# Kernel tuning notes

Measured on AMD Instinct MI355X. Metric: run time of the kernel, lower is better.

Reference implementation:

```python
import jax, jax.numpy as jnp
import numpy as np

EPS = 1e-5

def layer_norm(x, w, b):
    mu = jnp.mean(x, axis=-1, keepdims=True)
    var = jnp.mean(jnp.square(x - mu), axis=-1, keepdims=True)
    return (x - mu) * jax.lax.rsqrt(var + EPS) * w + b

def setup_inputs() -> dict:
    key = jax.random.key(0)
    ks = jax.random.split(key, 16)
    B, N, c_z, c_h = 1, 512, 128, 128
    s_z = 1.0 / np.sqrt(c_z)
    s_h = 1.0 / np.sqrt(c_h)
    return {
        "z": jax.random.normal(ks[0], (B, N, N, c_z), jnp.float32),
        "mask": jnp.ones((B, N, N), jnp.float32),
        "norm_in_w": jnp.ones((c_z,), jnp.float32),
        "norm_in_b": jnp.zeros((c_z,), jnp.float32),
        "a_p_w": jax.random.normal(ks[1], (c_h, c_z), jnp.float32) * s_z,
        "a_p_b": jnp.zeros((c_h,), jnp.float32),
        "a_g_w": jax.random.normal(ks[2], (c_h, c_z), jnp.float32) * s_z,
        "a_g_b": jnp.ones((c_h,), jnp.float32),
        "b_p_w": jax.random.normal(ks[3], (c_h, c_z), jnp.float32) * s_z,
        "b_p_b": jnp.zeros((c_h,), jnp.float32),
        "b_g_w": jax.random.normal(ks[4], (c_h, c_z), jnp.float32) * s_z,
        "b_g_b": jnp.ones((c_h,), jnp.float32),
        "g_w": jax.random.normal(ks[5], (c_z, c_z), jnp.float32) * s_z,
        "g_b": jnp.ones((c_z,), jnp.float32),
        "z_w": jax.random.normal(ks[6], (c_z, c_h), jnp.float32) * s_h,
        "z_b": jnp.zeros((c_z,), jnp.float32),
        "norm_out_w": jnp.ones((c_h,), jnp.float32),
        "norm_out_b": jnp.zeros((c_h,), jnp.float32),
    }

OUTGOING = True

def reference(z, mask, norm_in_w, norm_in_b, a_p_w, a_p_b, a_g_w, a_g_b,
              b_p_w, b_p_b, b_g_w, b_g_b, g_w, g_b, z_w, z_b,
              norm_out_w, norm_out_b):
    # z: [B, N, N, c_z]; mask: [B, N, N]
    m = mask[..., None]  # [B, N, N, 1]
    zn = layer_norm(z, norm_in_w, norm_in_b)
    # gated projections (nn.Linear layout: W is [out, in])
    a = m * jax.nn.sigmoid(zn @ a_g_w.T + a_g_b) * (zn @ a_p_w.T + a_p_b)
    b = m * jax.nn.sigmoid(zn @ b_g_w.T + b_g_b) * (zn @ b_p_w.T + b_p_b)
    if OUTGOING:
        # x[i,j,c] = sum_k a[i,k,c] * b[j,k,c]
        x = jnp.einsum('bikc,bjkc->bijc', a, b)
    else:
        x = jnp.einsum('bkic,bkjc->bijc', a, b)
    x = layer_norm(x, norm_out_w, norm_out_b)
    x = x @ z_w.T + z_b
    g = jax.nn.sigmoid(zn @ g_w.T + g_b)
    return x * g
```

## Files before the change

kernel.cpp:

```cpp
#include <hip/hip_runtime.h>
#include <stddef.h>

#define NN 512
#define CC 128
#define NPOS (NN*NN)
#define CPITCH (NPOS + 512)

typedef unsigned short u16;
typedef unsigned int   u32;
typedef u16  u16x4  __attribute__((ext_vector_type(4)));
typedef u16  u16x8  __attribute__((ext_vector_type(8)));
typedef __bf16 bf16x8 __attribute__((ext_vector_type(8)));
typedef float f32x4  __attribute__((ext_vector_type(4)));

__device__ __forceinline__ float b2f(u16 u) {
    union { u32 i; float f; } w; w.i = ((u32)u) << 16; return w.f;
}
__device__ __forceinline__ u16 f2b(float f) {
    return __builtin_bit_cast(u16, (__bf16)f);
}
__device__ __forceinline__ float sigm(float x) { return 1.0f / (1.0f + __expf(-x)); }

__device__ __forceinline__ void gld16(const u16* g, u16* l) {
    __builtin_amdgcn_global_load_lds(
        (const __attribute__((address_space(1))) u32*)g,
        (__attribute__((address_space(3))) u32*)l, 16, 0, 0);
}

struct W6 { const float* p[6]; };

__global__ __launch_bounds__(256) void k0_pack(W6 w, u16* __restrict__ dst)
{
    const int i = blockIdx.x * 256 + threadIdx.x;
    const int mt = i >> 14, r = i & 16383;
    const int cb = r >> 11, ks = (r >> 9) & 3, lane = (r >> 3) & 63, j = r & 7;
    const int row = cb * 16 + (lane & 15);
    const int col = ks * 32 + (lane >> 4) * 8 + j;
    dst[i] = f2b(w.p[mt][row * 128 + col]);
}

__global__ __launch_bounds__(128) void k1_ln_proj(
    const float* __restrict__ z,  const float* __restrict__ mask,
    const float* __restrict__ wi, const float* __restrict__ bi,
    const u16* __restrict__ wpk,
    const float* __restrict__ agb, const float* __restrict__ apb,
    const float* __restrict__ bgb, const float* __restrict__ bpb,
    u16* __restrict__ a_cm, u16* __restrict__ b_cm)
{
    __shared__ u16 zn[64][136];
    const int tid = threadIdx.x;
    const size_t p0 = (size_t)blockIdx.x * 64;

    {
        const float* zt = z + p0 * CC;
        const int g  = tid >> 5;
        const int c4 = (tid & 31) * 4;
        const f32x4 wi4 = *(const f32x4*)(wi + c4);
        const f32x4 bi4 = *(const f32x4*)(bi + c4);
        f32x4 v[16];
        #pragma unroll
        for (int h = 0; h < 16; ++h)
            v[h] = *(const f32x4*)(zt + h * 512 + tid * 4);
        #pragma unroll
        for (int h = 0; h < 16; ++h) {
            float s  = (v[h][0] + v[h][1]) + (v[h][2] + v[h][3]);
            float s2 = (v[h][0]*v[h][0] + v[h][1]*v[h][1])
                     + (v[h][2]*v[h][2] + v[h][3]*v[h][3]);
            #pragma unroll
            for (int ms = 1; ms <= 16; ms <<= 1) {
                s  += __shfl_xor(s,  ms);
                s2 += __shfl_xor(s2, ms);
            }
            const float mu   = s * (1.0f / CC);
            const float rstd = rsqrtf(s2 * (1.0f / CC) - mu * mu + 1e-5f);
            u16x4 o4;
            #pragma unroll
            for (int e = 0; e < 4; ++e) {
                const float nw = rstd * wi4[e];
                o4[e] = f2b(v[h][e] * nw + __builtin_fmaf(-mu, nw, bi4[e]));
            }
            *(u16x4*)&zn[h * 4 + g][c4] = o4;
        }
    }
    __syncthreads();

    const int wave = tid >> 6, lane = tid & 63;
    const int m = lane & 15, q = lane >> 4;

    bf16x8 af[2][4];
    #pragma unroll
    for (int t = 0; t < 2; ++t)
        #pragma unroll
        for (int ks = 0; ks < 4; ++ks)
            af[t][ks] = *(const bf16x8*)&zn[wave * 32 + t * 16 + m][ks * 32 + q * 8];

    f32x4 mkv[2];
    #pragma unroll
    for (int t = 0; t < 2; ++t)
        mkv[t] = *(const f32x4*)(mask + p0 + wave * 32 + t * 16 + q * 4);

    const float* Bv[4] = { agb, apb, bgb, bpb };

    for (int cb = 0; cb < 8; ++cb) {
        const int o = cb * 16 + m;
        f32x4 res[4][2];
        #pragma unroll
        for (int mt = 0; mt < 4; ++mt) {
            const float bvv = Bv[mt][o];
            #pragma unroll
            for (int t = 0; t < 2; ++t) res[mt][t] = f32x4{ bvv, bvv, bvv, bvv };
            const u16* wp = wpk + ((size_t)((mt * 8 + cb) * 4)) * 512 + (size_t)lane * 8;
            bf16x8 wf[4];
            #pragma unroll
            for (int ks = 0; ks < 4; ++ks) wf[ks] = *(const bf16x8*)(wp + ks * 512);
            #pragma unroll
            for (int ks = 0; ks < 4; ++ks)
                #pragma unroll
                for (int t = 0; t < 2; ++t)
                    res[mt][t] = __builtin_amdgcn_mfma_f32_16x16x32_bf16(
                                   af[t][ks], wf[ks], res[mt][t], 0, 0, 0);
        }
        #pragma unroll
        for (int t = 0; t < 2; ++t) {
            u16x4 av, bv;
            #pragma unroll
            for (int r = 0; r < 4; ++r) {
                const float mk = mkv[t][r];
                av[r] = f2b(mk * sigm(res[0][t][r]) * res[1][t][r]);
                bv[r] = f2b(mk * sigm(res[2][t][r]) * res[3][t][r]);
            }
            const size_t off = (size_t)o * CPITCH + p0 + wave * 32 + t * 16 + q * 4;
            *(u16x4*)(a_cm + off) = av;
            *(u16x4*)(b_cm + off) = bv;
        }
    }
}

__global__ __launch_bounds__(256) void k2_gemm(
    const u16* __restrict__ A, const u16* __restrict__ B, u16* __restrict__ X)
{
    __shared__ u16 As[2][128][32];
    __shared__ u16 Bs[2][128][32];
    const int tid = threadIdx.x;
    const int bx  = blockIdx.x;
    const int c   = bx >> 4;
    const int i0  = ((bx >> 2) & 3) * 128;
    const int j0  = (bx & 3) * 128;
    const size_t cbase = (size_t)c * CPITCH;
    const u16* Ac = A + cbase;
    const u16* Bc = B + cbase;

    const int wave = tid >> 6, lane = tid & 63;
    const int wm = wave >> 1, wn = wave & 1;
    const int m = lane & 15, q = lane >> 4;

    f32x4 acc[4][4];
    const f32x4 zero = { 0.f, 0.f, 0.f, 0.f };
    #pragma unroll
    for (int mt = 0; mt < 4; ++mt)
        #pragma unroll
        for (int nt = 0; nt < 4; ++nt) acc[mt][nt] = zero;

    for (int kt = 0; kt < 8; ++kt) {
        __syncthreads();
        #pragma unroll
        for (int ps = 0; ps < 4; ++ps) {
            const int id   = ps * 256 + tid;
            const int half = id >> 9;
            const int rw   = (id >> 2) & 127;
            const int g    = (id & 3) ^ ((rw >> 1) & 3);
            const size_t goff = (size_t)(kt * 64 + half * 32 + g * 8);
            gld16(Ac + (size_t)(i0 + rw) * NN + goff, &As[0][0][0] + id * 8);
            gld16(Bc + (size_t)(j0 + rw) * NN + goff, &Bs[0][0][0] + id * 8);
        }
        __syncthreads();
        #pragma unroll
        for (int ks = 0; ks < 2; ++ks) {
            bf16x8 af[4], bf[4];
            #pragma unroll
            for (int mt = 0; mt < 4; ++mt) {
                const int row = wm * 64 + mt * 16 + m;
                const int slot = q ^ ((row >> 1) & 3);
                af[mt] = *(const bf16x8*)&As[ks][row][slot * 8];
            }
            #pragma unroll
            for (int nt = 0; nt < 4; ++nt) {
                const int row = wn * 64 + nt * 16 + m;
                const int slot = q ^ ((row >> 1) & 3);
                bf[nt] = *(const bf16x8*)&Bs[ks][row][slot * 8];
            }
            #pragma unroll
            for (int mt = 0; mt < 4; ++mt)
                #pragma unroll
                for (int nt = 0; nt < 4; ++nt)
                    acc[mt][nt] = __builtin_amdgcn_mfma_f32_16x16x32_bf16(
                                    af[mt], bf[nt], acc[mt][nt], 0, 0, 0);
        }
    }

    #pragma unroll
    for (int mt = 0; mt < 4; ++mt) {
        #pragma unroll
        for (int r = 0; r < 4; ++r) {
            const int i = i0 + wm * 64 + mt * 16 + q * 4 + r;
            #pragma unroll
            for (int nt = 0; nt < 4; ++nt) {
                const int j = j0 + wn * 64 + nt * 16 + m;
                X[cbase + (size_t)i * NN + j] = f2b(acc[mt][nt][r]);
            }
        }
    }
}

__global__ __launch_bounds__(256) void k3_out(
    float* __restrict__ out, const u16* __restrict__ x_cm,
    const float* __restrict__ z,
    const float* __restrict__ wi, const float* __restrict__ bi,
    const float* __restrict__ wo, const float* __restrict__ bo,
    const u16* __restrict__ wpk,
    const float* __restrict__ gbv, const float* __restrict__ zbv)
{
    __shared__ u16 A[128][136];
    __shared__ u16 Bt[128][136];
    const int tid = threadIdx.x;
    const size_t p0 = (size_t)blockIdx.x * 128;
    const int wave = tid >> 6, lane = tid & 63;
    const int m = lane & 15, q = lane >> 4;
    const int pl = tid >> 1, ht = tid & 1;

    {
        const float* zr = z + (p0 + pl) * CC + ht * 64;
        float v[64];
        #pragma unroll
        for (int h = 0; h < 16; ++h) {
            f32x4 t = *(const f32x4*)(zr + h * 4);
            #pragma unroll
            for (int e = 0; e < 4; ++e) v[h * 4 + e] = t[e];
        }
        float s = 0.f, s2 = 0.f;
        #pragma unroll
        for (int e = 0; e < 64; ++e) { s += v[e]; s2 += v[e] * v[e]; }
        s  += __shfl_xor(s, 1);
        s2 += __shfl_xor(s2, 1);
        const float mu   = s * (1.0f / CC);
        const float rstd = rsqrtf(s2 * (1.0f / CC) - mu * mu + 1e-5f);
        #pragma unroll
        for (int h = 0; h < 8; ++h) {
            u16x8 o8;
            #pragma unroll
            for (int e = 0; e < 8; ++e) {
                const int c = ht * 64 + h * 8 + e;
                o8[e] = f2b((v[h * 8 + e] - mu) * rstd * wi[c] + bi[c]);
            }
            *(u16x8*)&A[pl][ht * 64 + h * 8] = o8;
        }
    }
    {
        const int c = tid >> 1, seg = tid & 1;
        #pragma unroll
        for (int e = 0; e < 8; ++e) {
            u16x8 vv = *(const u16x8*)(x_cm + (size_t)c * CPITCH + p0 + seg * 64 + e * 8);
            *(u16x8*)&Bt[c][seg * 64 + e * 8] = vv;
        }
    }
    __syncthreads();

    bf16x8 afz[2][4];
    #pragma unroll
    for (int t = 0; t < 2; ++t)
        #pragma unroll
        for (int ks = 0; ks < 4; ++ks)
            afz[t][ks] = *(const bf16x8*)&A[wave * 32 + t * 16 + m][ks * 32 + q * 8];
    __syncthreads();

    {
        float v[64];
        #pragma unroll
        for (int e = 0; e < 64; ++e) v[e] = b2f(Bt[ht * 64 + e][pl]);
        float s = 0.f, s2 = 0.f;
        #pragma unroll
        for (int e = 0; e < 64; ++e) { s += v[e]; s2 += v[e] * v[e]; }
        s  += __shfl_xor(s, 1);
        s2 += __shfl_xor(s2, 1);
        const float mu   = s * (1.0f / CC);
        const float rstd = rsqrtf(s2 * (1.0f / CC) - mu * mu + 1e-5f);
        #pragma unroll
        for (int h = 0; h < 8; ++h) {
            u16x8 o8;
            #pragma unroll
            for (int e = 0; e < 8; ++e) {
                const int c = ht * 64 + h * 8 + e;
                o8[e] = f2b((v[h * 8 + e] - mu) * rstd * wo[c] + bo[c]);
            }
            *(u16x8*)&A[pl][ht * 64 + h * 8] = o8;
        }
    }
    __syncthreads();

    bf16x8 afx[2][4];
    #pragma unroll
    for (int t = 0; t < 2; ++t)
        #pragma unroll
        for (int ks = 0; ks < 4; ++ks)
            afx[t][ks] = *(const bf16x8*)&A[wave * 32 + t * 16 + m][ks * 32 + q * 8];

    for (int cb = 0; cb < 8; ++cb) {
        const int o = cb * 16 + m;
        const float gb0 = gbv[o], zb0 = zbv[o];
        f32x4 accg[2], accx[2];
        #pragma unroll
        for (int t = 0; t < 2; ++t) {
            accg[t] = f32x4{ gb0, gb0, gb0, gb0 };
            accx[t] = f32x4{ zb0, zb0, zb0, zb0 };
        }
        const u16* wpg = wpk + ((size_t)((4 * 8 + cb) * 4)) * 512 + (size_t)lane * 8;
        const u16* wpz = wpk + ((size_t)((5 * 8 + cb) * 4)) * 512 + (size_t)lane * 8;
        bf16x8 wg[4], wz[4];
        #pragma unroll
        for (int ks = 0; ks < 4; ++ks) {
            wg[ks] = *(const bf16x8*)(wpg + ks * 512);
            wz[ks] = *(const bf16x8*)(wpz + ks * 512);
        }
        #pragma unroll
        for (int ks = 0; ks < 4; ++ks)
            #pragma unroll
            for (int t = 0; t < 2; ++t) {
                accg[t] = __builtin_amdgcn_mfma_f32_16x16x32_bf16(
                            afz[t][ks], wg[ks], accg[t], 0, 0, 0);
                accx[t] = __builtin_amdgcn_mfma_f32_16x16x32_bf16(
                            afx[t][ks], wz[ks], accx[t], 0, 0, 0);
            }
        #pragma unroll
        for (int t = 0; t < 2; ++t)
            #pragma unroll
            for (int r = 0; r < 4; ++r) {
                const size_t p = p0 + wave * 32 + t * 16 + q * 4 + r;
                out[p * CC + o] = accx[t][r] * sigm(accg[t][r]);
            }
    }
}

extern "C" void kernel_launch(void* const* d_in, const int* in_sizes, int n_in,
                              void* d_out, int out_size, void* d_ws, size_t ws_size,
                              hipStream_t stream)
{
    const float* z    = (const float*)d_in[0];
    const float* mask = (const float*)d_in[1];
    const float* wi   = (const float*)d_in[2];
    const float* bi   = (const float*)d_in[3];
    const float* apw  = (const float*)d_in[4];
    const float* apb  = (const float*)d_in[5];
    const float* agw  = (const float*)d_in[6];
    const float* agb  = (const float*)d_in[7];
    const float* bpw  = (const float*)d_in[8];
    const float* bpb  = (const float*)d_in[9];
    const float* bgw  = (const float*)d_in[10];
    const float* bgb  = (const float*)d_in[11];
    const float* gw   = (const float*)d_in[12];
    const float* gb   = (const float*)d_in[13];
    const float* zw   = (const float*)d_in[14];
    const float* zb   = (const float*)d_in[15];
    const float* wo   = (const float*)d_in[16];
    const float* bo   = (const float*)d_in[17];

    u16* a_cm = (u16*)d_ws;
    u16* b_cm = a_cm + (size_t)CC * CPITCH;
    u16* x_cm = b_cm + (size_t)CC * CPITCH;
    u16* w_pk = x_cm + (size_t)CC * CPITCH;
    float* out = (float*)d_out;

    W6 w6; w6.p[0] = agw; w6.p[1] = apw; w6.p[2] = bgw; w6.p[3] = bpw;
    w6.p[4] = gw; w6.p[5] = zw;

    k0_pack<<<6 * 16384 / 256, 256, 0, stream>>>(w6, w_pk);
    k1_ln_proj<<<NPOS / 64, 128, 0, stream>>>(z, mask, wi, bi, w_pk,
                                              agb, apb, bgb, bpb, a_cm, b_cm);
    k2_gemm<<<128 * 16, 256, 0, stream>>>(a_cm, b_cm, x_cm);
    k3_out<<<NPOS / 128, 256, 0, stream>>>(out, x_cm, z, wi, bi, wo, bo,
                                           w_pk, gb, zb);
}
```

Measured before the change: 492.9 us.

## Cache bf16 normalized z for output stage and remap GEMM blocks across XCDs

The projection kernel now also writes the layer-normalized input as bf16 in position-major layout to workspace. A new output kernel reads it directly instead of re-reading fp32 z and recomputing the input layernorm, which halves that read traffic and drops redundant math at the cost of an extra 64 MB write. Separately, the channel GEMM's block-to-work mapping is changed so consecutive blocks on the same XCD share a channel, meant to improve L2 locality. The old path is kept as a fallback when the workspace is too small.

Measured after the change: 480.5 us. -2.5%, faster.

```diff
diff --git a/kernel.cpp b/kernel.cpp
--- a/kernel.cpp
+++ b/kernel.cpp
@@ -45,7 +45,8 @@
     const u16* __restrict__ wpk,
     const float* __restrict__ agb, const float* __restrict__ apb,
     const float* __restrict__ bgb, const float* __restrict__ bpb,
-    u16* __restrict__ a_cm, u16* __restrict__ b_cm)
+    u16* __restrict__ a_cm, u16* __restrict__ b_cm,
+    u16* __restrict__ zn_pm)
 {
     __shared__ u16 zn[64][136];
     const int tid = threadIdx.x;
@@ -80,6 +81,8 @@
                 o4[e] = f2b(v[h][e] * nw + __builtin_fmaf(-mu, nw, bi4[e]));
             }
             *(u16x4*)&zn[h * 4 + g][c4] = o4;
+            if (zn_pm)
+                *(u16x4*)(zn_pm + (p0 + h * 4 + g) * CC + c4) = o4;
         }
     }
     __syncthreads();
@@ -143,9 +146,12 @@
     __shared__ u16 Bs[2][128][32];
     const int tid = threadIdx.x;
     const int bx  = blockIdx.x;
-    const int c   = bx >> 4;
-    const int i0  = ((bx >> 2) & 3) * 128;
-    const int j0  = (bx & 3) * 128;
+    const int xcd  = bx & 7;
+    const int slot = bx >> 3;
+    const int c    = (slot >> 4) * 8 + xcd;
+    const int tile = slot & 15;
+    const int i0   = (tile >> 2) * 128;
+    const int j0   = (tile & 3) * 128;
     const size_t cbase = (size_t)c * CPITCH;
     const u16* Ac = A + cbase;
     const u16* Bc = B + cbase;
@@ -180,14 +186,14 @@
             #pragma unroll
             for (int mt = 0; mt < 4; ++mt) {
                 const int row = wm * 64 + mt * 16 + m;
-                const int slot = q ^ ((row >> 1) & 3);
-                af[mt] = *(const bf16x8*)&As[ks][row][slot * 8];
+                const int slt = q ^ ((row >> 1) & 3);
+                af[mt] = *(const bf16x8*)&As[ks][row][slt * 8];
             }
             #pragma unroll
             for (int nt = 0; nt < 4; ++nt) {
                 const int row = wn * 64 + nt * 16 + m;
-                const int slot = q ^ ((row >> 1) & 3);
-                bf[nt] = *(const bf16x8*)&Bs[ks][row][slot * 8];
+                const int slt = q ^ ((row >> 1) & 3);
+                bf[nt] = *(const bf16x8*)&Bs[ks][row][slt * 8];
             }
             #pragma unroll
             for (int mt = 0; mt < 4; ++mt)
@@ -209,6 +215,105 @@
                 X[cbase + (size_t)i * NN + j] = f2b(acc[mt][nt][r]);
             }
         }
+    }
+}
+
+__global__ __launch_bounds__(256) void k3_out_zn(
+    float* __restrict__ out, const u16* __restrict__ x_cm,
+    const u16* __restrict__ zn_pm,
+    const float* __restrict__ wo, const float* __restrict__ bo,
+    const u16* __restrict__ wpk,
+    const float* __restrict__ gbv, const float* __restrict__ zbv)
+{
+    __shared__ u16 A[128][136];
+    __shared__ u16 Bt[128][136];
+    const int tid = threadIdx.x;
+    const size_t p0 = (size_t)blockIdx.x * 128;
+    const int wave = tid >> 6, lane = tid & 63;
+    const int m = lane & 15, q = lane >> 4;
+    const int pl = tid >> 1, ht = tid & 1;
+
+    {
+        const int c = tid >> 1, seg = tid & 1;
+        #pragma unroll
+        for (int e = 0; e < 8; ++e) {
+            u16x8 vv = *(const u16x8*)(x_cm + (size_t)c * CPITCH + p0 + seg * 64 + e * 8);
+            *(u16x8*)&Bt[c][seg * 64 + e * 8] = vv;
+        }
+    }
+    bf16x8 afz[2][4];
+    #pragma unroll
+    for (int t = 0; t < 2; ++t)
+        #pragma unroll
+        for (int ks = 0; ks < 4; ++ks)
+            afz[t][ks] = *(const bf16x8*)(zn_pm
+                           + (p0 + wave * 32 + t * 16 + m) * CC + ks * 32 + q * 8);
+    __syncthreads();
+
+    {
+        float v[64];
+        #pragma unroll
+        for (int e = 0; e < 64; ++e) v[e] = b2f(Bt[ht * 64 + e][pl]);
+        float s = 0.f, s2 = 0.f;
+        #pragma unroll
+        for (int e = 0; e < 64; ++e) { s += v[e]; s2 += v[e] * v[e]; }
+        s  += __shfl_xor(s, 1);
+        s2 += __shfl_xor(s2, 1);
+        const float mu   = s * (1.0f / CC);
+        const float rstd = rsqrtf(s2 * (1.0f / CC) - mu * mu + 1e-5f);
+        #pragma unroll
+        for (int h = 0; h < 8; ++h) {
+            u16x8 o8;
+            #pragma unroll
+            for (int e = 0; e < 8; ++e) {
+                const int c = ht * 64 + h * 8 + e;
+                o8[e] = f2b((v[h * 8 + e] - mu) * rstd * wo[c] + bo[c]);
+            }
+            *(u16x8*)&A[pl][ht * 64 + h * 8] = o8;
+        }
+    }
+    __syncthreads();
+
+    bf16x8 afx[2][4];
+    #pragma unroll
+    for (int t = 0; t < 2; ++t)
+        #pragma unroll
+        for (int ks = 0; ks < 4; ++ks)
+            afx[t][ks] = *(const bf16x8*)&A[wave * 32 + t * 16 + m][ks * 32 + q * 8];
+
+    for (int cb = 0; cb < 8; ++cb) {
+        const int o = cb * 16 + m;
+        const float gb0 = gbv[o], zb0 = zbv[o];
+        f32x4 accg[2], accx[2];
+        #pragma unroll
+        for (int t = 0; t < 2; ++t) {
+            accg[t] = f32x4{ gb0, gb0, gb0, gb0 };
+            accx[t] = f32x4{ zb0, zb0, zb0, zb0 };
+        }
+        const u16* wpg = wpk + ((size_t)((4 * 8 + cb) * 4)) * 512 + (size_t)lane * 8;
+        const u16* wpz = wpk + ((size_t)((5 * 8 + cb) * 4)) * 512 + (size_t)lane * 8;
+        bf16x8 wg[4], wz[4];
+        #pragma unroll
+        for (int ks = 0; ks < 4; ++ks) {
+            wg[ks] = *(const bf16x8*)(wpg + ks * 512);
+            wz[ks] = *(const bf16x8*)(wpz + ks * 512);
+        }
+        #pragma unroll
+        for (int ks = 0; ks < 4; ++ks)
+            #pragma unroll
+            for (int t = 0; t < 2; ++t) {
+                accg[t] = __builtin_amdgcn_mfma_f32_16x16x32_bf16(
+                            afz[t][ks], wg[ks], accg[t], 0, 0, 0);
+                accx[t] = __builtin_amdgcn_mfma_f32_16x16x32_bf16(
+                            afx[t][ks], wz[ks], accx[t], 0, 0, 0);
+            }
+        #pragma unroll
+        for (int t = 0; t < 2; ++t)
+            #pragma unroll
+            for (int r = 0; r < 4; ++r) {
+                const size_t p = p0 + wave * 32 + t * 16 + q * 4 + r;
+                out[p * CC + o] = accx[t][r] * sigm(accg[t][r]);
+            }
     }
 }
 
@@ -367,15 +472,25 @@
     u16* b_cm = a_cm + (size_t)CC * CPITCH;
     u16* x_cm = b_cm + (size_t)CC * CPITCH;
     u16* w_pk = x_cm + (size_t)CC * CPITCH;
+    u16* zn_pm = w_pk + (size_t)6 * 16384;
     float* out = (float*)d_out;
+
+    const size_t need_zn =
+        ((size_t)CC * CPITCH * 3 + 6 * 16384 + (size_t)NPOS * CC) * sizeof(u16);
+    const bool use_zn = (ws_size == 0) || (ws_size >= need_zn);
+    if (!use_zn) zn_pm = nullptr;
 
     W6 w6; w6.p[0] = agw; w6.p[1] = apw; w6.p[2] = bgw; w6.p[3] = bpw;
     w6.p[4] = gw; w6.p[5] = zw;
 
     k0_pack<<<6 * 16384 / 256, 256, 0, stream>>>(w6, w_pk);
     k1_ln_proj<<<NPOS / 64, 128, 0, stream>>>(z, mask, wi, bi, w_pk,
-                                              agb, apb, bgb, bpb, a_cm, b_cm);
+                                              agb, apb, bgb, bpb, a_cm, b_cm, zn_pm);
     k2_gemm<<<128 * 16, 256, 0, stream>>>(a_cm, b_cm, x_cm);
-    k3_out<<<NPOS / 128, 256, 0, stream>>>(out, x_cm, z, wi, bi, wo, bo,
-                                           w_pk, gb, zb);
-}
+    if (use_zn)
+        k3_out_zn<<<NPOS / 128, 256, 0, stream>>>(out, x_cm, zn_pm, wo, bo,
+                                                  w_pk, gb, zb);
+    else
+        k3_out<<<NPOS / 128, 256, 0, stream>>>(out, x_cm, z, wi, bi, wo, bo,
+                                               w_pk, gb, zb);
+}
```
